# Performance work log

Hardware: AMD Instinct MI355X
Metric: run time of the kernel (lower is better)

Reference implementation:

```python
import jax, jax.numpy as jnp
import numpy as np

B, S, D = 1, 2048, 512
H, KH, DH = 8, 2, 64
G = H // KH            # grouped queries per kv head
CBS = SBS = 32         # compress / selection block size (equal)
NSEL = 8               # num selected blocks
WIN = 128              # sliding window size
NC = S // CBS          # num compressed blocks
NF = S // SBS          # num fine blocks (S divisible by SBS)
CDIM = CBS * DH


def setup_inputs():
    key = jax.random.key(0)
    ks = jax.random.split(key, 12)
    r = lambda k, shape, s=0.02: jax.random.normal(k, shape, dtype=jnp.float32) * s
    return {
        "inp": jax.random.normal(ks[0], (B, S, D), dtype=jnp.float32),
        "norm_w": jnp.ones((D,), jnp.float32),
        "w_qkv": r(ks[1], (D, H * DH + 2 * KH * DH)),
        "mem_kv": r(ks[2], (2, KH, 1, DH)),
        "k_pos": r(ks[3], (KH, CBS, DH)),
        "v_pos": r(ks[4], (KH, CBS, DH)),
        "kc_w1": r(ks[5], (CDIM, CDIM)), "kc_b1": jnp.zeros((CDIM,), jnp.float32),
        "kc_w2": r(ks[6], (CDIM, DH)), "kc_b2": jnp.zeros((DH,), jnp.float32),
        "vc_w1": r(ks[7], (CDIM, CDIM)), "vc_b1": jnp.zeros((CDIM,), jnp.float32),
        "vc_w2": r(ks[8], (CDIM, DH)), "vc_b2": jnp.zeros((DH,), jnp.float32),
        "comb_w": r(ks[9], (D, 3 * H)),
        "comb_b": jnp.tile(jnp.array([-2.0, -2.0, 2.0], jnp.float32), H),
        "out_w": r(ks[10], (H * DH, D)),
    }


def _rope(x):  # x: [b, h, n, d]; interleaved rotary (rotary-embedding-torch style)
    d, n = x.shape[-1], x.shape[-2]
    inv = 1.0 / (10000.0 ** (jnp.arange(0, d, 2, dtype=jnp.float32) / d))
    fr = jnp.arange(n, dtype=jnp.float32)[:, None] * inv[None, :]  # [n, d/2]
    fr = jnp.repeat(fr, 2, axis=-1)                                 # [n, d]
    cos, sin = jnp.cos(fr), jnp.sin(fr)
    xp = x.reshape(*x.shape[:-1], d // 2, 2)
    xr = jnp.stack((-xp[..., 1], xp[..., 0]), axis=-1).reshape(x.shape)
    return x * cos + xr * sin


def _mlp(x, w1, b1, w2, b2):
    return jax.nn.relu(x @ w1 + b1) @ w2 + b2


def _forward(inp, norm_w, w_qkv, mem_kv, k_pos, v_pos, kc_w1, kc_b1, kc_w2, kc_b2,
             vc_w1, vc_b1, vc_w2, vc_b2, comb_w, comb_b, out_w):
    scale = DH ** -0.5
    NEG = -jnp.finfo(jnp.float32).max

    # RMSNorm
    x = inp * jax.lax.rsqrt(jnp.mean(inp * inp, -1, keepdims=True)
                            + jnp.finfo(jnp.float32).eps) * norm_w

    qkv = x @ w_qkv
    q, k, v = jnp.split(qkv, [H * DH, H * DH + KH * DH], axis=-1)
    q = q.reshape(B, S, H, DH).transpose(0, 2, 1, 3)    # b h n d
    k = k.reshape(B, S, KH, DH).transpose(0, 2, 1, 3)   # b kh n d
    v = v.reshape(B, S, KH, DH).transpose(0, 2, 1, 3)

    # --- 1. compressed attention (unrotated q/k) ---
    kb = k.reshape(B, KH, NC, CBS, DH) + k_pos[None, :, None]
    vb = v.reshape(B, KH, NC, CBS, DH) + v_pos[None, :, None]
    ck = _mlp(kb.reshape(B, KH, NC, CDIM), kc_w1, kc_b1, kc_w2, kc_b2)  # b kh nc d
    cv = _mlp(vb.reshape(B, KH, NC, CDIM), vc_w1, vc_b1, vc_w2, vc_b2)
    ck = jnp.concatenate((jnp.broadcast_to(mem_kv[0][None], (B, KH, 1, DH)), ck), axis=2)
    cv = jnp.concatenate((jnp.broadcast_to(mem_kv[1][None], (B, KH, 1, DH)), cv), axis=2)

    ck_pos = jnp.concatenate((jnp.array([-1]), (jnp.arange(NC) + 1) * CBS - 1))
    cmask = ck_pos[None, :] < jnp.arange(S)[:, None]     # [S, 1+NC]

    qg = q.reshape(B, KH, G, S, DH)
    csim = jnp.einsum('bhgid,bhjd->bhgij', qg, ck) * scale
    csim = jnp.where(cmask, csim, NEG)
    cattn = jax.nn.softmax(csim, axis=-1)
    c_out = jnp.einsum('bhgij,bhjd->bhgid', cattn, cv)   # b kh g n d

    # --- importance scores -> top-k block selection (shared across grouped queries) ---
    imp = csim[..., 1:].mean(axis=2)                     # b kh n nc
    imp = jnp.pad(imp, ((0, 0), (0, 0), (0, 0), (1, 0)), constant_values=-1e3)
    imp = jax.nn.softmax(imp, axis=-1)[..., 1:]
    sel_val, sel_idx = jax.lax.top_k(imp, NSEL)          # b kh n sel

    # --- rotary for fine + sliding branches ---
    qr, kr = _rope(q), _rope(k)

    # --- 2. fine (selected-block) attention ---
    own = jnp.broadcast_to((jnp.arange(S) // SBS)[None, None, :, None], (B, KH, S, 1))
    sel_idx = jnp.concatenate((sel_idx, own), axis=-1)   # b kh n (sel+1), own block appended

    bmask = jnp.broadcast_to((sel_val > 1e-10)[..., None], (B, KH, S, NSEL, SBS))
    tri = jnp.tril(jnp.ones((SBS, SBS), bool))
    diag = jnp.broadcast_to(jnp.tile(tri, (NF, 1))[None, None, :, None, :], (B, KH, S, 1, SBS))
    fmask = jnp.concatenate((bmask, diag), axis=-2).reshape(B, KH, 1, S, (NSEL + 1) * SBS)

    kfb = kr.reshape(B, KH, NF, SBS, DH)
    vfb = v.reshape(B, KH, NF, SBS, DH)
    gidx = sel_idx[..., None, None]                      # b kh n sel1 1 1
    fk = jnp.take_along_axis(kfb[:, :, None], gidx, axis=3).reshape(B, KH, S, (NSEL + 1) * SBS, DH)
    fv = jnp.take_along_axis(vfb[:, :, None], gidx, axis=3).reshape(B, KH, S, (NSEL + 1) * SBS, DH)

    fqg = qr.reshape(B, KH, G, S, DH)
    fsim = jnp.einsum('bhgid,bhijd->bhgij', fqg, fk) * scale
    fsim = jnp.where(fmask, fsim, NEG)
    fattn = jax.nn.softmax(fsim, axis=-1)
    f_out = jnp.einsum('bhgij,bhijd->bhgid', fattn, fv)  # b kh g n d

    diff = jnp.arange(S)[:, None] - jnp.arange(S)[None, :]
    smask = (diff >= 0) & (diff <= WIN)
    ssim = jnp.einsum('bhgid,bhjd->bhgij', fqg, kr) * scale
    ssim = jnp.where(smask, ssim, NEG)
    sattn = jax.nn.softmax(ssim, axis=-1)
    s_out = jnp.einsum('bhgij,bhjd->bhgid', sattn, v)    # b kh g n d

    # --- learned gating combine over [compressed, fine, sliding] ---
    gates = jax.nn.sigmoid(x @ comb_w + comb_b).reshape(B, S, H, 3)
    gates = gates.transpose(0, 2, 1, 3).reshape(B, KH, G, S, 3)
    out = gates[..., 0:1] * c_out + gates[..., 1:2] * f_out + gates[..., 2:3] * s_out
    out = out.reshape(B, H, S, DH).transpose(0, 2, 1, 3).reshape(B, S, H * DH)
    return out @ out_w


def reference(inp, norm_w, w_qkv, mem_kv, k_pos, v_pos, kc_w1, kc_b1, kc_w2, kc_b2,
              vc_w1, vc_b1, vc_w2, vc_b2, comb_w, comb_b, out_w):
    return _forward(inp, norm_w, w_qkv, mem_kv, k_pos, v_pos, kc_w1, kc_b1, kc_w2, kc_b2,
                    vc_w1, vc_b1, vc_w2, vc_b2, comb_w, comb_b, out_w)
```

## Files before the change

kernel.cpp:

```cpp
#include <hip/hip_runtime.h>
#include <hip/hip_bf16.h>
#include <math.h>

#define S 2048
#define D 512
#define H 8
#define KH 2
#define DH 64
#define G 4
#define CBS 32
#define NSEL 8
#define WIN 128
#define NC 64
#define CDIM 2048

typedef __attribute__((ext_vector_type(8))) short bf16x8_t;
typedef __attribute__((ext_vector_type(4))) float f32x4_t;
typedef __attribute__((ext_vector_type(2))) _Float16 half2v;

static __device__ __forceinline__ unsigned short f2bf(float f) {
    union { float f; unsigned int u; } v; v.f = f;
    unsigned int r = (v.u + 0x7FFFu + ((v.u >> 16) & 1u)) >> 16;
    return (unsigned short)r;
}
static __device__ __forceinline__ float bf2f(unsigned short h) {
    union { unsigned int u; float f; } v; v.u = ((unsigned int)h) << 16;
    return v.f;
}
static __device__ __forceinline__ float bflo(unsigned int u) {
    union { unsigned int u; float f; } v; v.u = u << 16; return v.f;
}
static __device__ __forceinline__ float bfhi(unsigned int u) {
    union { unsigned int u; float f; } v; v.u = u & 0xffff0000u; return v.f;
}
static __device__ __forceinline__ unsigned short f2h(float f) {
    union { _Float16 h; unsigned short s; } v; v.h = (_Float16)f; return v.s;
}
static __device__ __forceinline__ float h2f(unsigned short u) {
    union { unsigned short s; _Float16 h; } v; v.s = u; return (float)v.h;
}
static __device__ __forceinline__ float dot2f16(unsigned int a, unsigned int b, float c) {
    union { unsigned int u; half2v h; } A, B; A.u = a; B.u = b;
    return __builtin_amdgcn_fdot2(A.h, B.h, c, false);
}

__global__ __launch_bounds__(256) void k_prep(const float* __restrict__ inp,
                                              const float* __restrict__ w,
                                              unsigned short* __restrict__ xbf,
                                              float* __restrict__ ct, float* __restrict__ st) {
    int b = blockIdx.x, t = threadIdx.x;
    if (b < S) {
        const float* row = inp + (size_t)b * D;
        float a = row[t], c = row[t + 256];
        float ss = a * a + c * c;
        for (int off = 32; off; off >>= 1) ss += __shfl_xor(ss, off);
        __shared__ float red[4];
        if ((t & 63) == 0) red[t >> 6] = ss;
        __syncthreads();
        float tot = red[0] + red[1] + red[2] + red[3];
        float inv = rsqrtf(tot / (float)D + 1.1920929e-07f);
        xbf[(size_t)b * D + t]       = f2bf(a * inv * w[t]);
        xbf[(size_t)b * D + t + 256] = f2bf(c * inv * w[t + 256]);
    } else {
        int idx = (b - S) * 256 + t;
        int s = idx >> 5, p = idx & 31;
        float inv = powf(10000.0f, -(float)p / 32.0f);
        float fr = (float)s * inv;
        ct[idx] = cosf(fr); st[idx] = sinf(fr);
    }
}

__global__ __launch_bounds__(256) void k_gemm0(
    const unsigned short* __restrict__ A,
    const float* __restrict__ W,
    const float* __restrict__ k_pos, const float* __restrict__ v_pos,
    const float* __restrict__ ct, const float* __restrict__ st,
    unsigned short* __restrict__ q16,
    unsigned short* __restrict__ qr16, unsigned short* __restrict__ kr16,
    unsigned short* __restrict__ v16, unsigned short* __restrict__ kbvb)
{
    const int K = 512, N = 768;
    __shared__ __align__(16) unsigned short As[64][40];
    __shared__ __align__(16) unsigned short Bs[64][40];
    int t = threadIdx.x;
    int m0 = blockIdx.y * 64, n0 = blockIdx.x * 64;
    int wave = t >> 6, lane = t & 63;
    int mh = wave & 1, nh = wave >> 1;
    f32x4_t acc[2][2] = {};
    int ar = t >> 2, ac = (t & 3) * 8;
    int bk = t >> 3, bn = (t & 7) * 8;
    int arow_l = lane & 15, kcol = (lane >> 4) * 8;
    uint4 aReg = *(const uint4*)&A[(size_t)(m0 + ar) * K + ac];
    const float4* wr = (const float4*)&W[(size_t)bk * N + n0 + bn];
    float4 w0 = wr[0], w1 = wr[1];
    for (int k0 = 0; k0 < K; k0 += 32) {
        __syncthreads();
        *(uint4*)&As[ar][ac] = aReg;
        unsigned short bp[8];
        bp[0] = f2bf(w0.x); bp[1] = f2bf(w0.y); bp[2] = f2bf(w0.z); bp[3] = f2bf(w0.w);
        bp[4] = f2bf(w1.x); bp[5] = f2bf(w1.y); bp[6] = f2bf(w1.z); bp[7] = f2bf(w1.w);
        #pragma unroll
        for (int j = 0; j < 8; ++j) Bs[bn + j][bk] = bp[j];
        __syncthreads();
        if (k0 + 32 < K) {
            aReg = *(const uint4*)&A[(size_t)(m0 + ar) * K + k0 + 32 + ac];
            wr = (const float4*)&W[(size_t)(k0 + 32 + bk) * N + n0 + bn];
            w0 = wr[0]; w1 = wr[1];
        }
        bf16x8_t a0 = *(const bf16x8_t*)&As[mh * 32 + arow_l][kcol];
        bf16x8_t a1 = *(const bf16x8_t*)&As[mh * 32 + 16 + arow_l][kcol];
        bf16x8_t b0v = *(const bf16x8_t*)&Bs[nh * 32 + arow_l][kcol];
        bf16x8_t b1v = *(const bf16x8_t*)&Bs[nh * 32 + 16 + arow_l][kcol];
        acc[0][0] = __builtin_amdgcn_mfma_f32_16x16x32_bf16(a0, b0v, acc[0][0], 0, 0, 0);
        acc[0][1] = __builtin_amdgcn_mfma_f32_16x16x32_bf16(a0, b1v, acc[0][1], 0, 0, 0);
        acc[1][0] = __builtin_amdgcn_mfma_f32_16x16x32_bf16(a1, b0v, acc[1][0], 0, 0, 0);
        acc[1][1] = __builtin_amdgcn_mfma_f32_16x16x32_bf16(a1, b1v, acc[1][1], 0, 0, 0);
    }
    #pragma unroll
    for (int mi = 0; mi < 2; ++mi)
    #pragma unroll
    for (int ni = 0; ni < 2; ++ni)
    #pragma unroll
    for (int r = 0; r < 4; ++r) {
        int gm = m0 + mh * 32 + mi * 16 + (lane >> 4) * 4 + r;
        int gn = n0 + nh * 32 + ni * 16 + (lane & 15);
        float val = acc[mi][ni][r];
        float part = __shfl_xor(val, 1);
        if (gn < 512) {
            int hh = gn >> 6, d = gn & 63;
            size_t idx = ((size_t)hh * S + gm) * DH + d;
            q16[idx] = f2h(val);
            int p = d >> 1;
            float cc = ct[gm * 32 + p], sn = st[gm * 32 + p];
            float y = (d & 1) ? (val * cc + part * sn) : (val * cc - part * sn);
            qr16[idx] = f2h(y);
        } else if (gn < 640) {
            int gk = gn - 512, khh = gk >> 6, d = gk & 63;
            size_t idx = ((size_t)khh * S + gm) * DH + d;
            int p = d >> 1;
            float cc = ct[gm * 32 + p], sn = st[gm * 32 + p];
            float y = (d & 1) ? (val * cc + part * sn) : (val * cc - part * sn);
            kr16[idx] = f2h(y);
            int tt = gm & 31, nc2 = gm >> 5;
            kbvb[((size_t)(khh * 64 + nc2)) * 2048 + tt * 64 + d] =
                f2bf(val + k_pos[(khh * CBS + tt) * 64 + d]);
        } else {
            int gv = gn - 640, khh = gv >> 6, d = gv & 63;
            size_t idx = ((size_t)khh * S + gm) * DH + d;
            v16[idx] = f2bf(val);
            int tt = gm & 31, nc2 = gm >> 5;
            kbvb[((size_t)(128 + khh * 64 + nc2)) * 2048 + tt * 64 + d] =
                f2bf(val + v_pos[(khh * CBS + tt) * 64 + d]);
        }
    }
}

template<int MODE>
__global__ __launch_bounds__(256) void k_gemm(
    const unsigned short* __restrict__ A,
    const float* __restrict__ B0,
    int M, int N, int K,
    float* __restrict__ outC)
{
    __shared__ __align__(16) unsigned short As[64][40];
    __shared__ __align__(16) unsigned short Bs[64][40];
    int t = threadIdx.x;
    int m0 = blockIdx.y * 64, n0 = blockIdx.x * 64;
    const float* W = B0;
    int wave = t >> 6, lane = t & 63;
    int mh = wave & 1, nh = wave >> 1;
    f32x4_t acc[2][2] = {};
    int ar = t >> 2, ac = (t & 3) * 8;
    int bk = t >> 3, bn = (t & 7) * 8;
    int arow_l = lane & 15, kcol = (lane >> 4) * 8;
    uint4 aReg = *(const uint4*)&A[(size_t)(m0 + ar) * K + ac];
    const float4* wr = (const float4*)&W[(size_t)bk * N + n0 + bn];
    float4 w0 = wr[0], w1 = wr[1];
    for (int k0 = 0; k0 < K; k0 += 32) {
        __syncthreads();
        *(uint4*)&As[ar][ac] = aReg;
        unsigned short bp[8];
        bp[0] = f2bf(w0.x); bp[1] = f2bf(w0.y); bp[2] = f2bf(w0.z); bp[3] = f2bf(w0.w);
        bp[4] = f2bf(w1.x); bp[5] = f2bf(w1.y); bp[6] = f2bf(w1.z); bp[7] = f2bf(w1.w);
        #pragma unroll
        for (int j = 0; j < 8; ++j) Bs[bn + j][bk] = bp[j];
        __syncthreads();
        if (k0 + 32 < K) {
            aReg = *(const uint4*)&A[(size_t)(m0 + ar) * K + k0 + 32 + ac];
            wr = (const float4*)&W[(size_t)(k0 + 32 + bk) * N + n0 + bn];
            w0 = wr[0]; w1 = wr[1];
        }
        bf16x8_t a0 = *(const bf16x8_t*)&As[mh * 32 + arow_l][kcol];
        bf16x8_t a1 = *(const bf16x8_t*)&As[mh * 32 + 16 + arow_l][kcol];
        bf16x8_t b0v = *(const bf16x8_t*)&Bs[nh * 32 + arow_l][kcol];
        bf16x8_t b1v = *(const bf16x8_t*)&Bs[nh * 32 + 16 + arow_l][kcol];
        acc[0][0] = __builtin_amdgcn_mfma_f32_16x16x32_bf16(a0, b0v, acc[0][0], 0, 0, 0);
        acc[0][1] = __builtin_amdgcn_mfma_f32_16x16x32_bf16(a0, b1v, acc[0][1], 0, 0, 0);
        acc[1][0] = __builtin_amdgcn_mfma_f32_16x16x32_bf16(a1, b0v, acc[1][0], 0, 0, 0);
        acc[1][1] = __builtin_amdgcn_mfma_f32_16x16x32_bf16(a1, b1v, acc[1][1], 0, 0, 0);
    }
    #pragma unroll
    for (int mi = 0; mi < 2; ++mi)
    #pragma unroll
    for (int ni = 0; ni < 2; ++ni)
    #pragma unroll
    for (int r = 0; r < 4; ++r) {
        int gm = m0 + mh * 32 + mi * 16 + (lane >> 4) * 4 + r;
        int gn = n0 + nh * 32 + ni * 16 + (lane & 15);
        outC[(size_t)gm * N + gn] = acc[mi][ni][r];
    }
}

__global__ __launch_bounds__(256) void k_gemm1p(
    const unsigned short* __restrict__ A,
    const float* __restrict__ kc_w1, const float* __restrict__ vc_w1,
    float* __restrict__ part)
{
    const int N = 2048, LDA = 2048;
    __shared__ __align__(16) unsigned short As[64][40];
    __shared__ __align__(16) unsigned short Bs[64][40];
    int t = threadIdx.x;
    int mb = blockIdx.y & 3, ks = blockIdx.y >> 2;
    int m0 = mb * 64, n0 = blockIdx.x * 64, kbeg = ks * 1024;
    const float* W = (mb >= 2) ? vc_w1 : kc_w1;
    int wave = t >> 6, lane = t & 63;
    int mh = wave & 1, nh = wave >> 1;
    f32x4_t acc[2][2] = {};
    int ar = t >> 2, ac = (t & 3) * 8;
    int bk = t >> 3, bn = (t & 7) * 8;
    int arow_l = lane & 15, kcol = (lane >> 4) * 8;
    uint4 aReg = *(const uint4*)&A[(size_t)(m0 + ar) * LDA + kbeg + ac];
    const float4* wr = (const float4*)&W[(size_t)(kbeg + bk) * N + n0 + bn];
    float4 w0 = wr[0], w1 = wr[1];
    for (int k0 = 0; k0 < 1024; k0 += 32) {
        __syncthreads();
        *(uint4*)&As[ar][ac] = aReg;
        unsigned short bp[8];
        bp[0] = f2bf(w0.x); bp[1] = f2bf(w0.y); bp[2] = f2bf(w0.z); bp[3] = f2bf(w0.w);
        bp[4] = f2bf(w1.x); bp[5] = f2bf(w1.y); bp[6] = f2bf(w1.z); bp[7] = f2bf(w1.w);
        #pragma unroll
        for (int j = 0; j < 8; ++j) Bs[bn + j][bk] = bp[j];
        __syncthreads();
        if (k0 + 32 < 1024) {
            aReg = *(const uint4*)&A[(size_t)(m0 + ar) * LDA + kbeg + k0 + 32 + ac];
            wr = (const float4*)&W[(size_t)(kbeg + k0 + 32 + bk) * N + n0 + bn];
            w0 = wr[0]; w1 = wr[1];
        }
        bf16x8_t a0 = *(const bf16x8_t*)&As[mh * 32 + arow_l][kcol];
        bf16x8_t a1 = *(const bf16x8_t*)&As[mh * 32 + 16 + arow_l][kcol];
        bf16x8_t b0v = *(const bf16x8_t*)&Bs[nh * 32 + arow_l][kcol];
        bf16x8_t b1v = *(const bf16x8_t*)&Bs[nh * 32 + 16 + arow_l][kcol];
        acc[0][0] = __builtin_amdgcn_mfma_f32_16x16x32_bf16(a0, b0v, acc[0][0], 0, 0, 0);
        acc[0][1] = __builtin_amdgcn_mfma_f32_16x16x32_bf16(a0, b1v, acc[0][1], 0, 0, 0);
        acc[1][0] = __builtin_amdgcn_mfma_f32_16x16x32_bf16(a1, b0v, acc[1][0], 0, 0, 0);
        acc[1][1] = __builtin_amdgcn_mfma_f32_16x16x32_bf16(a1, b1v, acc[1][1], 0, 0, 0);
    }
    #pragma unroll
    for (int mi = 0; mi < 2; ++mi)
    #pragma unroll
    for (int ni = 0; ni < 2; ++ni)
    #pragma unroll
    for (int r = 0; r < 4; ++r) {
        int gm = m0 + mh * 32 + mi * 16 + (lane >> 4) * 4 + r;
        int gn = n0 + nh * 32 + ni * 16 + (lane & 15);
        part[((size_t)ks * 256 + gm) * N + gn] = acc[mi][ni][r];
    }
}

__global__ __launch_bounds__(256) void k_gemm1r(
    const float4* __restrict__ part, const float* __restrict__ kc_b1,
    const float* __restrict__ vc_b1, uint2* __restrict__ hid)
{
    int idx = blockIdx.x * 256 + threadIdx.x;
    int gm = idx >> 9, gn4 = (idx & 511) * 4;
    float4 a = part[idx], b = part[idx + 131072];
    const float* bias = (gm >= 128) ? vc_b1 : kc_b1;
    float r0 = fmaxf(a.x + b.x + bias[gn4 + 0], 0.f);
    float r1 = fmaxf(a.y + b.y + bias[gn4 + 1], 0.f);
    float r2 = fmaxf(a.z + b.z + bias[gn4 + 2], 0.f);
    float r3 = fmaxf(a.w + b.w + bias[gn4 + 3], 0.f);
    uint2 o;
    o.x = (unsigned)f2bf(r0) | ((unsigned)f2bf(r1) << 16);
    o.y = (unsigned)f2bf(r2) | ((unsigned)f2bf(r3) << 16);
    hid[idx] = o;
}

__global__ __launch_bounds__(256) void k_mlp2p(
    const unsigned short* __restrict__ A,
    const float* __restrict__ kc_w2, const float* __restrict__ vc_w2,
    float* __restrict__ part)
{
    const int N = 64, LDA = 2048;
    __shared__ __align__(16) unsigned short As[64][40];
    __shared__ __align__(16) unsigned short Bs[64][40];
    int t = threadIdx.x;
    int ks = blockIdx.x, m0 = blockIdx.y * 64;
    int kbeg = ks * 512;
    const float* W = (blockIdx.y >= 2) ? vc_w2 : kc_w2;
    int wave = t >> 6, lane = t & 63;
    int mh = wave & 1, nh = wave >> 1;
    f32x4_t acc[2][2] = {};
    int ar = t >> 2, ac = (t & 3) * 8;
    int bk = t >> 3, bn = (t & 7) * 8;
    int arow_l = lane & 15, kcol = (lane >> 4) * 8;
    uint4 aReg = *(const uint4*)&A[(size_t)(m0 + ar) * LDA + kbeg + ac];
    const float4* wr = (const float4*)&W[(size_t)(kbeg + bk) * N + bn];
    float4 w0 = wr[0], w1 = wr[1];
    for (int k0 = 0; k0 < 512; k0 += 32) {
        __syncthreads();
        *(uint4*)&As[ar][ac] = aReg;
        unsigned short bp[8];
        bp[0] = f2bf(w0.x); bp[1] = f2bf(w0.y); bp[2] = f2bf(w0.z); bp[3] = f2bf(w0.w);
        bp[4] = f2bf(w1.x); bp[5] = f2bf(w1.y); bp[6] = f2bf(w1.z); bp[7] = f2bf(w1.w);
        #pragma unroll
        for (int j = 0; j < 8; ++j) Bs[bn + j][bk] = bp[j];
        __syncthreads();
        if (k0 + 32 < 512) {
            aReg = *(const uint4*)&A[(size_t)(m0 + ar) * LDA + kbeg + k0 + 32 + ac];
            wr = (const float4*)&W[(size_t)(kbeg + k0 + 32 + bk) * N + bn];
            w0 = wr[0]; w1 = wr[1];
        }
        bf16x8_t a0 = *(const bf16x8_t*)&As[mh * 32 + arow_l][kcol];
        bf16x8_t a1 = *(const bf16x8_t*)&As[mh * 32 + 16 + arow_l][kcol];
        bf16x8_t b0v = *(const bf16x8_t*)&Bs[nh * 32 + arow_l][kcol];
        bf16x8_t b1v = *(const bf16x8_t*)&Bs[nh * 32 + 16 + arow_l][kcol];
        acc[0][0] = __builtin_amdgcn_mfma_f32_16x16x32_bf16(a0, b0v, acc[0][0], 0, 0, 0);
        acc[0][1] = __builtin_amdgcn_mfma_f32_16x16x32_bf16(a0, b1v, acc[0][1], 0, 0, 0);
        acc[1][0] = __builtin_amdgcn_mfma_f32_16x16x32_bf16(a1, b0v, acc[1][0], 0, 0, 0);
        acc[1][1] = __builtin_amdgcn_mfma_f32_16x16x32_bf16(a1, b1v, acc[1][1], 0, 0, 0);
    }
    #pragma unroll
    for (int mi = 0; mi < 2; ++mi)
    #pragma unroll
    for (int ni = 0; ni < 2; ++ni)
    #pragma unroll
    for (int r = 0; r < 4; ++r) {
        int gm = m0 + mh * 32 + mi * 16 + (lane >> 4) * 4 + r;
        int gn = nh * 32 + ni * 16 + (lane & 15);
        part[((size_t)ks * 256 + gm) * 64 + gn] = acc[mi][ni][r];
    }
}

__global__ __launch_bounds__(256) void k_mlp2r(
    const float* __restrict__ part, const float* __restrict__ kc_b2,
    const float* __restrict__ vc_b2, const float* __restrict__ mem_kv,
    unsigned short* __restrict__ ck16, float* __restrict__ cv)
{
    int idx = blockIdx.x * 256 + threadIdx.x;
    int gm = idx >> 6, gn = idx & 63;
    float sum = part[(size_t)gm * 64 + gn] + part[(size_t)(256 + gm) * 64 + gn]
              + part[(size_t)(512 + gm) * 64 + gn] + part[(size_t)(768 + gm) * 64 + gn];
    bool isv = gm >= 128;
    sum += isv ? vc_b2[gn] : kc_b2[gn];
    int kh2 = (gm >> 6) & 1, nc2 = gm & 63;
    if (isv) cv[(kh2 * 65 + 1 + nc2) * 64 + gn] = sum;
    else     ck16[(kh2 * 65 + 1 + nc2) * 64 + gn] = f2h(sum);
    if (blockIdx.x == 0 && threadIdx.x < 256) {
        int t = threadIdx.x;
        int path2 = t >> 7, khm = (t >> 6) & 1, dm = t & 63;
        float mv = mem_kv[path2 * (KH * DH) + khm * DH + dm];
        if (path2) cv[khm * 65 * 64 + dm] = mv;
        else       ck16[khm * 65 * 64 + dm] = f2h(mv);
    }
}

__global__ __launch_bounds__(256) void k_cattn(
    const unsigned short* __restrict__ q16, const unsigned short* __restrict__ ck16,
    const float* __restrict__ cv,
    float* __restrict__ c_out, int* __restrict__ sel)
{
    int kh = blockIdx.x >> 9, sc = blockIdx.x & 511;
    int s_base = sc * 4;
    __shared__ __align__(16) unsigned char KL[64 * 128];
    __shared__ float cvL[64][66];
    __shared__ unsigned short qL16[4][64];
    __shared__ float simL[4][64];
    __shared__ float pL[4][64];
    int t = threadIdx.x;
    {
        int j = t >> 2, gp = (t & 3) * 2;
        const uint4* src = (const uint4*)&ck16[((size_t)kh * 65 + j) * 64];
        uint4 a = src[gp], b = src[gp + 1];
        *(uint4*)(KL + j * 128 + 16 * (gp ^ (j & 7)))       = a;
        *(uint4*)(KL + j * 128 + 16 * ((gp + 1) ^ (j & 7))) = b;
    }
    for (int idx = t; idx < 4096; idx += 256) {
        int j = idx >> 6, d = idx & 63;
        cvL[j][d] = cv[(kh * 65 + j) * 64 + d];
    }
    int g = t >> 6, lane = t & 63;
    for (int si = 0; si < 4; ++si) {
        int s = s_base + si;
        __syncthreads();
        qL16[g][lane] = q16[((kh * G + g) * S + s) * DH + lane];
        __syncthreads();
        int j = lane;
        bool valid = (j == 0) || (s >= j * 32);
        float sva = 0.f, svb = 0.f, svc = 0.f, svd = 0.f;
        #pragma unroll
        for (int grp = 0; grp < 8; ++grp) {
            uint4 kk = *(const uint4*)(KL + j * 128 + 16 * (grp ^ (j & 7)));
            uint4 qq = *(const uint4*)((const unsigned char*)qL16 + g * 128 + 16 * grp);
            sva = dot2f16(kk.x, qq.x, sva);
            svb = dot2f16(kk.y, qq.y, svb);
            svc = dot2f16(kk.z, qq.z, svc);
            svd = dot2f16(kk.w, qq.w, svd);
        }
        float sim = ((sva + svb) + (svc + svd)) * 0.125f;
        float simm = valid ? sim : -INFINITY;
        simL[g][j] = simm;
        float m = simm;
        for (int off = 32; off; off >>= 1) m = fmaxf(m, __shfl_xor(m, off));
        float p = valid ? __expf(simm - m) : 0.f;
        float den = p;
        for (int off = 32; off; off >>= 1) den += __shfl_xor(den, off);
        pL[g][j] = p / den;
        float acc = 0.f;
        #pragma unroll
        for (int j4 = 0; j4 < 16; ++j4) {
            float4 p4 = *(const float4*)&pL[g][j4 * 4];
            acc += p4.x * cvL[j4 * 4 + 0][lane] + p4.y * cvL[j4 * 4 + 1][lane]
                 + p4.z * cvL[j4 * 4 + 2][lane] + p4.w * cvL[j4 * 4 + 3][lane];
        }
        c_out[((kh * G + g) * S + s) * DH + lane] = acc;
        __syncthreads();
        if (g == 0) {
            int l = lane;
            float lv = -INFINITY;
            if (l < 63 && s >= (l + 1) * 32)
                lv = 0.25f * (simL[0][l + 1] + simL[1][l + 1] + simL[2][l + 1] + simL[3][l + 1]);
            float mm = lv;
            for (int off = 32; off; off >>= 1) mm = fmaxf(mm, __shfl_xor(mm, off));
            mm = fmaxf(mm, -1000.0f);
            float e = (lv == -INFINITY) ? 0.f : __expf(lv - mm);
            float dd = e;
            for (int off = 32; off; off >>= 1) dd += __shfl_xor(dd, off);
            dd += __expf(-1000.0f - mm);
            float val = e / dd;
            float vc = val;
            int base = (kh * S + s) * 9;
            for (int t8 = 0; t8 < 8; ++t8) {
                float bv2 = vc; int bi = l;
                for (int off = 32; off; off >>= 1) {
                    float ov = __shfl_xor(bv2, off); int oi = __shfl_xor(bi, off);
                    if (ov > bv2 || (ov == bv2 && oi < bi)) { bv2 = ov; bi = oi; }
                }
                if (l == 0) sel[base + t8] = (bv2 > 1e-10f) ? bi : -1;
                if (l == bi) vc = -1.f;
            }
            if (l == 0) sel[base + 8] = s >> 5;
        }
    }
}

__global__ __launch_bounds__(256, 4) void k_swattn(
    const unsigned short* __restrict__ qr16, const unsigned short* __restrict__ kr16,
    const unsigned short* __restrict__ v16, const int* __restrict__ sel,
    float* __restrict__ fob, float* __restrict__ sob)
{
    int kh = blockIdx.x >> 11, s = blockIdx.x & 2047;
    int t = threadIdx.x, w = t >> 6, lane = t & 63, g = w;
    __shared__ __align__(16) unsigned char KL[2][64 * 128];
    __shared__ __align__(16) unsigned char VL[2][64 * 144];
    __shared__ float pL[4][64];

    const uint4* qp = (const uint4*)&qr16[(((size_t)kh * G + g) * S + s) * DH];
    uint4 qq0 = qp[0], qq1 = qp[1], qq2 = qp[2], qq3 = qp[3];
    uint4 qq4 = qp[4], qq5 = qp[5], qq6 = qp[6], qq7 = qp[7];

    int base = (kh * S + s) * 9;
    int lo = s - WIN; if (lo < 0) lo = 0;

    int nv = 0;
    #pragma unroll
    for (int i = 0; i < 8; ++i) nv += (sel[base + i] >= 0) ? 1 : 0;
    int npairF = (nv + 1) >> 1;
    int nchS = (s - lo + 63) >> 6;
    int nch = npairF + nchS;
    int ownStart = s & ~31;
    bool hasOwn = (s & 31) != 0;

    float lF = 0.f, lS = 0.f;
    float a0F = 0.f, a1F = 0.f, a0S = 0.f, a1S = 0.f;
    int h = lane >> 5, dhalf = lane & 31;
    int key = w * 16 + (lane & 15);
    int grpA = lane >> 4;
    uint4 z = make_uint4(0, 0, 0, 0);
    uint4 kd0 = z, kd1 = z, vd0 = z, vd1 = z;

    auto issue = [&](int c) {
        int gkey; bool kv;
        if (c < npairF) {
            int b = sel[base + 2 * c + ((key >> 5) & 1)];
            kv = b >= 0;
            gkey = (kv ? b : 0) * 32 + (key & 31);
        } else {
            gkey = lo + (c - npairF) * 64 + key;
            kv = gkey < s;
        }
        const uint4* kp = (const uint4*)&kr16[((size_t)kh * S + gkey) * DH];
        const uint4* vp = (const uint4*)&v16 [((size_t)kh * S + gkey) * DH];
        kd0 = kv ? kp[grpA] : z;
        kd1 = kv ? kp[grpA + 4] : z;
        vd0 = kv ? vp[grpA] : z;
        vd1 = kv ? vp[grpA + 4] : z;
    };
    auto stage = [&](int buf) {
        *(uint4*)(KL[buf] + key * 128 + 16 * (grpA ^ (key & 7))) = kd0;
        *(uint4*)(KL[buf] + key * 128 + 16 * ((grpA + 4) ^ (key & 7))) = kd1;
        *(uint4*)(VL[buf] + key * 144 + 16 * grpA) = vd0;
        *(uint4*)(VL[buf] + key * 144 + 16 * (grpA + 4)) = vd1;
    };

    issue(0);
    stage(0);
    if (nch > 1) issue(1);
    __syncthreads();

    for (int c = 0; c < nch; ++c) {
        const unsigned char* KLc = KL[c & 1];
        const unsigned char* VLc = VL[c & 1];

        int j = lane;
        bool isPair = c < npairF;
        int cs = c - npairF;
        int gk0 = lo + cs * 64;
        bool valid = isPair ? ((j < 32) || ((2 * c + 1) < nv))
                            : ((gk0 + j) < s);

        float sva = 0.f, svb = 0.f, svc = 0.f, svd = 0.f;
        #define QKSTEP(G_, QQ_) { \
            uint4 kk = *(const uint4*)(KLc + j * 128 + 16 * ((G_) ^ (j & 7))); \
            sva = dot2f16(kk.x, QQ_.x, sva); svb = dot2f16(kk.y, QQ_.y, svb); \
            svc = dot2f16(kk.z, QQ_.z, svc); svd = dot2f16(kk.w, QQ_.w, svd); }
        QKSTEP(0, qq0) QKSTEP(1, qq1) QKSTEP(2, qq2) QKSTEP(3, qq3)
        QKSTEP(4, qq4) QKSTEP(5, qq5) QKSTEP(6, qq6) QKSTEP(7, qq7)
        #undef QKSTEP
        float sv = (sva + svb) + (svc + svd);
        float p = valid ? __expf(sv * 0.125f) : 0.f;
        pL[g][j] = p;

        bool doOwn = (!isPair) && hasOwn && (cs == nchS - 1);
        if (!doOwn) {
            if (isPair) lF += p; else lS += p;
            float t0 = 0.f, t1 = 0.f;
            #pragma unroll
            for (int j4 = 0; j4 < 8; ++j4) {
                float4 p4 = *(const float4*)&pL[g][h * 32 + j4 * 4];
                const float* pp = (const float*)&p4;
                #pragma unroll
                for (int q2 = 0; q2 < 4; ++q2) {
                    unsigned int v2 = *(const unsigned int*)(VLc + (h * 32 + j4 * 4 + q2) * 144 + 4 * dhalf);
                    t0 += pp[q2] * bflo(v2);
                    t1 += pp[q2] * bfhi(v2);
                }
            }
            if (isPair) { a0F += t0; a1F += t1; }
            else        { a0S += t0; a1S += t1; }
        } else {
            lS += p;
            int jstart = ownStart - gk0;
            if (j >= jstart) lF += p;
            float pre0 = 0.f, pre1 = 0.f, suf0 = 0.f, suf1 = 0.f;
            #pragma unroll
            for (int j4 = 0; j4 < 8; ++j4) {
                float4 p4 = *(const float4*)&pL[g][h * 32 + j4 * 4];
                const float* pp = (const float*)&p4;
                #pragma unroll
                for (int q2 = 0; q2 < 4; ++q2) {
                    int jj = h * 32 + j4 * 4 + q2;
                    unsigned int v2 = *(const unsigned int*)(VLc + jj * 144 + 4 * dhalf);
                    float t0 = pp[q2] * bflo(v2);
                    float t1 = pp[q2] * bfhi(v2);
                    bool inSuf = jj >= jstart;
                    suf0 += inSuf ? t0 : 0.f;
                    suf1 += inSuf ? t1 : 0.f;
                    pre0 += inSuf ? 0.f : t0;
                    pre1 += inSuf ? 0.f : t1;
                }
            }
            a0S += pre0 + suf0; a1S += pre1 + suf1;
            a0F += suf0;        a1F += suf1;
        }

        if (c + 1 < nch) {
            stage((c + 1) & 1);
            if (c + 2 < nch) issue(c + 2);
        }
        __syncthreads();
    }
    {
        float qd = h2f(qr16[(((size_t)kh * G + g) * S + s) * DH + lane]);
        float pr = qd * h2f(kr16[((size_t)kh * S + s) * DH + lane]);
        for (int off = 32; off; off >>= 1) pr += __shfl_xor(pr, off);
        float pd = __expf(pr * 0.125f);
        for (int off = 32; off; off >>= 1) {
            lF += __shfl_xor(lF, off);
            lS += __shfl_xor(lS, off);
        }
        lF += pd; lS += pd;
        if (h == 0) {
            unsigned int v2 = *(const unsigned int*)&v16[(((size_t)kh * S + s) * DH) + 2 * dhalf];
            float b0 = bflo(v2), b1 = bfhi(v2);
            a0F += pd * b0; a1F += pd * b1;
            a0S += pd * b0; a1S += pd * b1;
        }
    }
    a0F += __shfl_xor(a0F, 32);
    a1F += __shfl_xor(a1F, 32);
    a0S += __shfl_xor(a0S, 32);
    a1S += __shfl_xor(a1S, 32);
    if (lane < 32) {
        size_t ob = (((size_t)kh * G + g) * S + s) * DH + 2 * dhalf;
        float invF = 1.f / lF, invS = 1.f / lS;
        *(float2*)&fob[ob] = make_float2(a0F * invF, a1F * invF);
        *(float2*)&sob[ob] = make_float2(a0S * invS, a1S * invS);
    }
}

__global__ __launch_bounds__(256) void k_combine(
    const unsigned short* __restrict__ xbf, const float* __restrict__ comb_w, const float* __restrict__ comb_b,
    const float* __restrict__ c_out, const float* __restrict__ f_out, const float* __restrict__ s_out,
    unsigned short* __restrict__ comb)
{
    int s = blockIdx.x, t = threadIdx.x;
    __shared__ float gpart[24][8];
    __shared__ float gates[24];
    if (t < 192) {
        int cc = t >> 3, pt = t & 7;
        float sum = 0.f;
        for (int d = pt * 64; d < pt * 64 + 64; ++d)
            sum += bf2f(xbf[s * D + d]) * comb_w[d * 24 + cc];
        gpart[cc][pt] = sum;
    }
    __syncthreads();
    if (t < 24) {
        float sum = comb_b[t];
        for (int i = 0; i < 8; ++i) sum += gpart[t][i];
        gates[t] = 1.f / (1.f + __expf(-sum));
    }
    __syncthreads();
    for (int o = t; o < 512; o += 256) {
        int h = o >> 6, d = o & 63;
        int idx = (h * S + s) * DH + d;
        float r = gates[h * 3] * c_out[idx] + gates[h * 3 + 1] * f_out[idx] + gates[h * 3 + 2] * s_out[idx];
        comb[s * D + o] = f2bf(r);
    }
}

extern "C" void kernel_launch(void* const* d_in, const int* in_sizes, int n_in,
                              void* d_out, int out_size, void* d_ws, size_t ws_size,
                              hipStream_t stream)
{
    (void)in_sizes; (void)n_in; (void)out_size; (void)ws_size;
    const float* inp    = (const float*)d_in[0];
    const float* norm_w = (const float*)d_in[1];
    const float* w_qkv  = (const float*)d_in[2];
    const float* mem_kv = (const float*)d_in[3];
    const float* k_pos  = (const float*)d_in[4];
    const float* v_pos  = (const float*)d_in[5];
    const float* kc_w1  = (const float*)d_in[6];
    const float* kc_b1  = (const float*)d_in[7];
    const float* kc_w2  = (const float*)d_in[8];
    const float* kc_b2  = (const float*)d_in[9];
    const float* vc_w1  = (const float*)d_in[10];
    const float* vc_b1  = (const float*)d_in[11];
    const float* vc_w2  = (const float*)d_in[12];
    const float* vc_b2  = (const float*)d_in[13];
    const float* comb_w = (const float*)d_in[14];
    const float* comb_b = (const float*)d_in[15];
    const float* out_w  = (const float*)d_in[16];
    float* out = (float*)d_out;

    char* w = (char*)d_ws;
    size_t off = 0;
    auto alloc = [&](size_t bytes) { void* p = w + off; off += (bytes + 255) & ~(size_t)255; return p; };
    unsigned short* xbf   = (unsigned short*)alloc((size_t)S * D * 2);
    unsigned short* kbvb  = (unsigned short*)alloc((size_t)256 * 2048 * 2);
    unsigned short* hid   = (unsigned short*)alloc((size_t)256 * 2048 * 2);
    unsigned short* combb = (unsigned short*)alloc((size_t)S * 512 * 2);
    unsigned short* q16   = (unsigned short*)alloc((size_t)H * S * DH * 2);
    unsigned short* qr16  = (unsigned short*)alloc((size_t)H * S * DH * 2);
    unsigned short* kr16  = (unsigned short*)alloc((size_t)KH * S * DH * 2);
    unsigned short* v16   = (unsigned short*)alloc((size_t)KH * S * DH * 2);
    unsigned short* ck16  = (unsigned short*)alloc((size_t)KH * 65 * 64 * 2);
    float* cvb  = (float*)alloc((size_t)KH * 65 * 64 * 4);
    float* cob  = (float*)alloc((size_t)H * S * DH * 4);
    float* fob  = (float*)alloc((size_t)H * S * DH * 4);
    float* sob  = (float*)alloc((size_t)H * S * DH * 4);
    float* ctab = (float*)alloc((size_t)S * 32 * 4);
    float* stab = (float*)alloc((size_t)S * 32 * 4);
    float* partb = (float*)alloc((size_t)4 * 256 * 64 * 4);
    float* g1part = (float*)alloc((size_t)2 * 256 * 2048 * 4);
    int*   selb = (int*)alloc((size_t)KH * S * 9 * 4);

    k_prep<<<S + 256, 256, 0, stream>>>(inp, norm_w, xbf, ctab, stab);

    k_gemm0<<<dim3(768 / 64, S / 64), 256, 0, stream>>>(
        xbf, w_qkv, k_pos, v_pos, ctab, stab, q16, qr16, kr16, v16, kbvb);

    k_gemm1p<<<dim3(32, 8), 256, 0, stream>>>(kbvb, kc_w1, vc_w1, g1part);
    k_gemm1r<<<512, 256, 0, stream>>>((const float4*)g1part, kc_b1, vc_b1, (uint2*)hid);

    k_mlp2p<<<dim3(4, 4), 256, 0, stream>>>(hid, kc_w2, vc_w2, partb);
    k_mlp2r<<<64, 256, 0, stream>>>(partb, kc_b2, vc_b2, mem_kv, ck16, cvb);

    k_cattn<<<KH * 512, 256, 0, stream>>>(q16, ck16, cvb, cob, selb);

    k_swattn<<<KH * S, 256, 0, stream>>>(qr16, kr16, v16, selb, fob, sob);

    k_combine<<<S, 256, 0, stream>>>(xbf, comb_w, comb_b, cob, fob, sob, combb);
    k_gemm<2><<<dim3(512 / 64, S / 64), 256, 0, stream>>>(
        combb, out_w, S, 512, 512, out);
}
```

Baseline: 213.7 us.

## Fuse split-K reduce into MLP2 GEMM and parallelize top-k selection in cattn

Removes the k_gemm1r kernel. k_mlp2p now reads the two fp32 split-K partials directly, adds the bias, applies ReLU and converts to bf16 while staging into shared memory, which saves one launch and the bf16 hidden-buffer round trip. In k_cattn the four query rows are prefetched into registers up front, dropping two barriers per row. The serial 8-round shuffle-based top-k is replaced by a one-pass rank count in which each lane compares itself against all 64 scores in shared memory. The trade-off is that k_mlp2p, with only 16 blocks, now reads twice as many fp32 bytes for its A operand.

```diff
diff --git a/kernel.cpp b/kernel.cpp
--- a/kernel.cpp
+++ b/kernel.cpp
@@ -267,26 +267,9 @@
     }
 }
 
-__global__ __launch_bounds__(256) void k_gemm1r(
-    const float4* __restrict__ part, const float* __restrict__ kc_b1,
-    const float* __restrict__ vc_b1, uint2* __restrict__ hid)
-{
-    int idx = blockIdx.x * 256 + threadIdx.x;
-    int gm = idx >> 9, gn4 = (idx & 511) * 4;
-    float4 a = part[idx], b = part[idx + 131072];
-    const float* bias = (gm >= 128) ? vc_b1 : kc_b1;
-    float r0 = fmaxf(a.x + b.x + bias[gn4 + 0], 0.f);
-    float r1 = fmaxf(a.y + b.y + bias[gn4 + 1], 0.f);
-    float r2 = fmaxf(a.z + b.z + bias[gn4 + 2], 0.f);
-    float r3 = fmaxf(a.w + b.w + bias[gn4 + 3], 0.f);
-    uint2 o;
-    o.x = (unsigned)f2bf(r0) | ((unsigned)f2bf(r1) << 16);
-    o.y = (unsigned)f2bf(r2) | ((unsigned)f2bf(r3) << 16);
-    hid[idx] = o;
-}
-
 __global__ __launch_bounds__(256) void k_mlp2p(
-    const unsigned short* __restrict__ A,
+    const float* __restrict__ g1part,
+    const float* __restrict__ kc_b1, const float* __restrict__ vc_b1,
     const float* __restrict__ kc_w2, const float* __restrict__ vc_w2,
     float* __restrict__ part)
 {
@@ -296,19 +279,35 @@
     int t = threadIdx.x;
     int ks = blockIdx.x, m0 = blockIdx.y * 64;
     int kbeg = ks * 512;
-    const float* W = (blockIdx.y >= 2) ? vc_w2 : kc_w2;
+    const float* W  = (blockIdx.y >= 2) ? vc_w2 : kc_w2;
+    const float* b1 = (m0 >= 128) ? vc_b1 : kc_b1;
     int wave = t >> 6, lane = t & 63;
     int mh = wave & 1, nh = wave >> 1;
     f32x4_t acc[2][2] = {};
     int ar = t >> 2, ac = (t & 3) * 8;
     int bk = t >> 3, bn = (t & 7) * 8;
     int arow_l = lane & 15, kcol = (lane >> 4) * 8;
-    uint4 aReg = *(const uint4*)&A[(size_t)(m0 + ar) * LDA + kbeg + ac];
+    int arow = m0 + ar;
+    const float4* p0 = (const float4*)&g1part[(size_t)arow * LDA + kbeg + ac];
+    const float4* p1 = (const float4*)&g1part[(size_t)(256 + arow) * LDA + kbeg + ac];
+    const float4* bb = (const float4*)&b1[kbeg + ac];
+    float4 x0 = p0[0], x1 = p0[1], y0 = p1[0], y1 = p1[1], c0 = bb[0], c1 = bb[1];
     const float4* wr = (const float4*)&W[(size_t)(kbeg + bk) * N + bn];
     float4 w0 = wr[0], w1 = wr[1];
     for (int k0 = 0; k0 < 512; k0 += 32) {
         __syncthreads();
-        *(uint4*)&As[ar][ac] = aReg;
+        {
+            unsigned short ap[8];
+            ap[0] = f2bf(fmaxf(x0.x + y0.x + c0.x, 0.f));
+            ap[1] = f2bf(fmaxf(x0.y + y0.y + c0.y, 0.f));
+            ap[2] = f2bf(fmaxf(x0.z + y0.z + c0.z, 0.f));
+            ap[3] = f2bf(fmaxf(x0.w + y0.w + c0.w, 0.f));
+            ap[4] = f2bf(fmaxf(x1.x + y1.x + c1.x, 0.f));
+            ap[5] = f2bf(fmaxf(x1.y + y1.y + c1.y, 0.f));
+            ap[6] = f2bf(fmaxf(x1.z + y1.z + c1.z, 0.f));
+            ap[7] = f2bf(fmaxf(x1.w + y1.w + c1.w, 0.f));
+            *(uint4*)&As[ar][ac] = *(const uint4*)ap;
+        }
         unsigned short bp[8];
         bp[0] = f2bf(w0.x); bp[1] = f2bf(w0.y); bp[2] = f2bf(w0.z); bp[3] = f2bf(w0.w);
         bp[4] = f2bf(w1.x); bp[5] = f2bf(w1.y); bp[6] = f2bf(w1.z); bp[7] = f2bf(w1.w);
@@ -316,7 +315,11 @@
         for (int j = 0; j < 8; ++j) Bs[bn + j][bk] = bp[j];
         __syncthreads();
         if (k0 + 32 < 512) {
-            aReg = *(const uint4*)&A[(size_t)(m0 + ar) * LDA + kbeg + k0 + 32 + ac];
+            int kk2 = kbeg + k0 + 32 + ac;
+            p0 = (const float4*)&g1part[(size_t)arow * LDA + kk2];
+            p1 = (const float4*)&g1part[(size_t)(256 + arow) * LDA + kk2];
+            bb = (const float4*)&b1[kk2];
+            x0 = p0[0]; x1 = p0[1]; y0 = p1[0]; y1 = p1[1]; c0 = bb[0]; c1 = bb[1];
             wr = (const float4*)&W[(size_t)(kbeg + k0 + 32 + bk) * N + bn];
             w0 = wr[0]; w1 = wr[1];
         }
@@ -377,6 +380,11 @@
     __shared__ float simL[4][64];
     __shared__ float pL[4][64];
     int t = threadIdx.x;
+    int g = t >> 6, lane = t & 63;
+    unsigned short qv0 = q16[((kh * G + g) * S + s_base + 0) * DH + lane];
+    unsigned short qv1 = q16[((kh * G + g) * S + s_base + 1) * DH + lane];
+    unsigned short qv2 = q16[((kh * G + g) * S + s_base + 2) * DH + lane];
+    unsigned short qv3 = q16[((kh * G + g) * S + s_base + 3) * DH + lane];
     {
         int j = t >> 2, gp = (t & 3) * 2;
         const uint4* src = (const uint4*)&ck16[((size_t)kh * 65 + j) * 64];
@@ -388,12 +396,10 @@
         int j = idx >> 6, d = idx & 63;
         cvL[j][d] = cv[(kh * 65 + j) * 64 + d];
     }
-    int g = t >> 6, lane = t & 63;
+    __syncthreads();
     for (int si = 0; si < 4; ++si) {
         int s = s_base + si;
-        __syncthreads();
-        qL16[g][lane] = q16[((kh * G + g) * S + s) * DH + lane];
-        __syncthreads();
+        qL16[g][lane] = (si == 0) ? qv0 : (si == 1) ? qv1 : (si == 2) ? qv2 : qv3;
         int j = lane;
         bool valid = (j == 0) || (s >= j * 32);
         float sva = 0.f, svb = 0.f, svc = 0.f, svd = 0.f;
@@ -437,19 +443,23 @@
             for (int off = 32; off; off >>= 1) dd += __shfl_xor(dd, off);
             dd += __expf(-1000.0f - mm);
             float val = e / dd;
-            float vc = val;
+            pL[0][l] = val;
+            int rk = 0;
+            #pragma unroll
+            for (int j4 = 0; j4 < 16; ++j4) {
+                float4 v4 = *(const float4*)&pL[0][j4 * 4];
+                const float* vv = (const float*)&v4;
+                #pragma unroll
+                for (int q2 = 0; q2 < 4; ++q2) {
+                    int i2 = j4 * 4 + q2;
+                    rk += (vv[q2] > val || (vv[q2] == val && i2 < l)) ? 1 : 0;
+                }
+            }
             int base = (kh * S + s) * 9;
-            for (int t8 = 0; t8 < 8; ++t8) {
-                float bv2 = vc; int bi = l;
-                for (int off = 32; off; off >>= 1) {
-                    float ov = __shfl_xor(bv2, off); int oi = __shfl_xor(bi, off);
-                    if (ov > bv2 || (ov == bv2 && oi < bi)) { bv2 = ov; bi = oi; }
-                }
-                if (l == 0) sel[base + t8] = (bv2 > 1e-10f) ? bi : -1;
-                if (l == bi) vc = -1.f;
-            }
+            if (rk < 8) sel[base + rk] = (val > 1e-10f) ? l : -1;
             if (l == 0) sel[base + 8] = s >> 5;
         }
+        __syncthreads();
     }
 }
 
@@ -677,7 +687,6 @@
     auto alloc = [&](size_t bytes) { void* p = w + off; off += (bytes + 255) & ~(size_t)255; return p; };
     unsigned short* xbf   = (unsigned short*)alloc((size_t)S * D * 2);
     unsigned short* kbvb  = (unsigned short*)alloc((size_t)256 * 2048 * 2);
-    unsigned short* hid   = (unsigned short*)alloc((size_t)256 * 2048 * 2);
     unsigned short* combb = (unsigned short*)alloc((size_t)S * 512 * 2);
     unsigned short* q16   = (unsigned short*)alloc((size_t)H * S * DH * 2);
     unsigned short* qr16  = (unsigned short*)alloc((size_t)H * S * DH * 2);
@@ -700,9 +709,8 @@
         xbf, w_qkv, k_pos, v_pos, ctab, stab, q16, qr16, kr16, v16, kbvb);
 
     k_gemm1p<<<dim3(32, 8), 256, 0, stream>>>(kbvb, kc_w1, vc_w1, g1part);
-    k_gemm1r<<<512, 256, 0, stream>>>((const float4*)g1part, kc_b1, vc_b1, (uint2*)hid);
-
-    k_mlp2p<<<dim3(4, 4), 256, 0, stream>>>(hid, kc_w2, vc_w2, partb);
+
+    k_mlp2p<<<dim3(4, 4), 256, 0, stream>>>(g1part, kc_b1, vc_b1, kc_w2, vc_w2, partb);
     k_mlp2r<<<64, 256, 0, stream>>>(partb, kc_b2, vc_b2, mem_kv, ck16, cvb);
 
     k_cattn<<<KH * 512, 256, 0, stream>>>(q16, ck16, cvb, cob, selb);
```

Result: faster. 202.6 us, median of 4 (-5.2%).
